# Optimization experiments

Measured on AMD Instinct MI355X. Metric: run time of the kernel, lower is better.

The kernel has to match this reference:

```python
import jax, jax.numpy as jnp
import numpy as np

NUM_HEADS = 16
D_MODEL = 1024
TEMPERATURE = D_MODEL ** 0.5  # note: module uses d_model**0.5, not head_dim**0.5


def setup_inputs() -> dict:
    key = jax.random.key(0)
    ks = jax.random.split(key, 8)
    B, T, D = 2, 2048, D_MODEL
    q = jax.random.normal(ks[0], (B, T, D), dtype=jnp.float32)
    k = jax.random.normal(ks[1], (B, T, D), dtype=jnp.float32)
    v = jax.random.normal(ks[2], (B, T, D), dtype=jnp.float32)
    # causal mask (tril) as suggested by the module docstring
    mask = jnp.tril(jnp.ones((T, T), dtype=bool))
    s = 1.0 / np.sqrt(D)
    Wq = jax.random.normal(ks[3], (D, D), dtype=jnp.float32) * s
    Wk = jax.random.normal(ks[4], (D, D), dtype=jnp.float32) * s
    Wv = jax.random.normal(ks[5], (D, D), dtype=jnp.float32) * s
    Wc = jax.random.normal(ks[6], (D, D), dtype=jnp.float32) * s
    return {"q": q, "k": k, "v": v, "Wq": Wq, "Wk": Wk, "Wv": Wv, "Wc": Wc, "mask": mask}


def reference(q, k, v, Wq, Wk, Wv, Wc, mask):
    B, T, D = q.shape
    H = NUM_HEADS
    hd = D // H
    # torch Linear (no bias): y = x @ W.T ; then split heads -> [B,H,T,hd]
    def proj(x, W):
        return (x @ W.T).reshape(B, T, H, hd).transpose(0, 2, 1, 3)
    qh, kh, vh = proj(q, Wq), proj(k, Wk), proj(v, Wv)
    # scores [B,H,T,T]
    scores = jnp.einsum("bhqd,bhkd->bhqk", qh / TEMPERATURE, kh)
    scores = jnp.where(mask, scores, -jnp.inf)
    attention = jax.nn.softmax(scores, axis=-1)  # dropout = identity (eval)
    out = jnp.einsum("bhqk,bhkd->bhqd", attention, vh)
    out = out.transpose(0, 2, 1, 3).reshape(B, T, D)
    out = out @ Wc.T  # combine projection; dropout = identity (eval)
    return (out, attention)
```

## Files before the change

kernel.cpp:

```cpp
#include <hip/hip_runtime.h>
#include <stdint.h>

typedef unsigned short u16;
typedef __bf16 bf16x8 __attribute__((ext_vector_type(8)));
typedef float f32x4 __attribute__((ext_vector_type(4)));

#define MFMA16(a, b, c) __builtin_amdgcn_mfma_f32_16x16x32_bf16((a), (b), (c), 0, 0, 0)

__device__ __forceinline__ u16 f2bf(float f) {
  union { __bf16 h; u16 u; } v;
  v.h = (__bf16)f;
  return v.u;
}

__device__ __forceinline__ float expf_c(float x) {
  return __expf(fmaxf(x, -80.0f));
}

__device__ __forceinline__ void gl_lds16(const u16* g, u16* l) {
  __builtin_amdgcn_global_load_lds(
      (const __attribute__((address_space(1))) unsigned int*)g,
      (__attribute__((address_space(3))) unsigned int*)l, 16, 0, 0);
}

struct Cvt6Args {
  const float* s0; const float* s1; const float* s2;
  const float* s3; const float* s4; const float* s5;
  u16* d0; u16* d1; u16* d2; u16* d3; u16* d4; u16* d5;
};

__global__ __launch_bounds__(256) void cvt6(Cvt6Args a) {
  const int z = blockIdx.y;
  const float* s; u16* d; int n8;
  if (z == 0)      { s = a.s0; d = a.d0; n8 = (4 * 1024 * 1024) / 8; }
  else if (z == 1) { s = a.s1; d = a.d1; n8 = (4 * 1024 * 1024) / 8; }
  else if (z == 2) { s = a.s2; d = a.d2; n8 = (4 * 1024 * 1024) / 8; }
  else if (z == 3) { s = a.s3; d = a.d3; n8 = (1024 * 1024) / 8; }
  else if (z == 4) { s = a.s4; d = a.d4; n8 = (1024 * 1024) / 8; }
  else             { s = a.s5; d = a.d5; n8 = (1024 * 1024) / 8; }
  const int i = blockIdx.x * 256 + threadIdx.x;
  if (i >= n8) return;
  float4 f0 = ((const float4*)s)[2 * i];
  float4 f1 = ((const float4*)s)[2 * i + 1];
  ushort4 h0, h1;
  h0.x = f2bf(f0.x); h0.y = f2bf(f0.y); h0.z = f2bf(f0.z); h0.w = f2bf(f0.w);
  h1.x = f2bf(f1.x); h1.y = f2bf(f1.y); h1.z = f2bf(f1.z); h1.w = f2bf(f1.w);
  ((ushort4*)d)[2 * i] = h0;
  ((ushort4*)d)[2 * i + 1] = h1;
}

__global__ __launch_bounds__(256) void cvt_one(const float* __restrict__ s,
                                               u16* __restrict__ d) {
  const int i = blockIdx.x * 256 + threadIdx.x;
  if (i >= (1024 * 1024) / 8) return;
  float4 f0 = ((const float4*)s)[2 * i];
  float4 f1 = ((const float4*)s)[2 * i + 1];
  ushort4 h0, h1;
  h0.x = f2bf(f0.x); h0.y = f2bf(f0.y); h0.z = f2bf(f0.z); h0.w = f2bf(f0.w);
  h1.x = f2bf(f1.x); h1.y = f2bf(f1.y); h1.z = f2bf(f1.z); h1.w = f2bf(f1.w);
  ((ushort4*)d)[2 * i] = h0;
  ((ushort4*)d)[2 * i + 1] = h1;
}

template <int BM>
__device__ __forceinline__ void gemm_core(const u16* __restrict__ X,
                                          const u16* __restrict__ W,
                                          void* __restrict__ Yv, float scale,
                                          int omode) {
  constexpr int NF = (BM == 128) ? 4 : 2;
  constexpr int ASEG = BM / 8;
  constexpr int CNT = (ASEG + 16) / 4;
  __shared__ __align__(16) u16 lA[BM * 64];
  __shared__ __align__(16) u16 lB[128 * 64];
  const int tid = threadIdx.x;
  const int lane = tid & 63, w = tid >> 6;
  const int l15 = lane & 15, quad = lane >> 4;
  const int wm = (BM == 128) ? (w >> 1) * 64 : 0;
  const int wn = (BM == 128) ? (w & 1) * 64 : w * 32;
  const int n0 = blockIdx.x * 128, m0 = blockIdx.y * BM;

  f32x4 acc[4][NF];
#pragma unroll
  for (int m = 0; m < 4; ++m)
#pragma unroll
    for (int n = 0; n < NF; ++n) acc[m][n] = (f32x4){0.f, 0.f, 0.f, 0.f};

  const int row8 = lane >> 3;
  const int slot = lane & 7;
  const int scol = ((slot ^ row8) << 3);

  for (int kk = 0; kk < 1024; kk += 64) {
    __syncthreads();
#pragma unroll
    for (int ps = 0; ps < CNT; ++ps) {
      const int s = w * CNT + ps;
      if (s < ASEG) {
        const int row = s * 8 + row8;
        gl_lds16(&X[(size_t)(m0 + row) * 1024 + kk + scol], &lA[s * 512]);
      } else {
        const int s2 = s - ASEG;
        const int row = s2 * 8 + row8;
        gl_lds16(&W[(size_t)(n0 + row) * 1024 + kk + scol], &lB[s2 * 512]);
      }
    }
    __syncthreads();
    bf16x8 af[2][4], bfr[2][NF];
#pragma unroll
    for (int h = 0; h < 2; ++h) {
#pragma unroll
      for (int m = 0; m < 4; ++m) {
        const int rA = wm + m * 16 + l15;
        af[h][m] = *(const bf16x8*)&lA[rA * 64 + (((quad + 4 * h) ^ (rA & 7)) << 3)];
      }
#pragma unroll
      for (int n = 0; n < NF; ++n) {
        const int rB = wn + n * 16 + l15;
        bfr[h][n] = *(const bf16x8*)&lB[rB * 64 + (((quad + 4 * h) ^ (rB & 7)) << 3)];
      }
    }
#pragma unroll
    for (int h = 0; h < 2; ++h)
#pragma unroll
      for (int m = 0; m < 4; ++m)
#pragma unroll
        for (int n = 0; n < NF; ++n)
          acc[m][n] = MFMA16(af[h][m], bfr[h][n], acc[m][n]);
  }

  if (omode == 0) {
    u16* Y = (u16*)Yv;
#pragma unroll
    for (int m = 0; m < 4; ++m) {
      int grow0 = m0 + wm + m * 16 + quad * 4;
#pragma unroll
      for (int n = 0; n < NF; ++n) {
        int gcol = n0 + wn + n * 16 + l15;
#pragma unroll
        for (int r = 0; r < 4; ++r)
          Y[(size_t)(grow0 + r) * 1024 + gcol] = f2bf(acc[m][n][r] * scale);
      }
    }
  } else if (omode == 1) {
    u16* Y = (u16*)Yv;
#pragma unroll
    for (int m = 0; m < 4; ++m) {
      int grow0 = m0 + wm + m * 16 + quad * 4;
      int bb = grow0 >> 11, t = grow0 & 2047;
#pragma unroll
      for (int n = 0; n < NF; ++n) {
        int gcol = n0 + wn + n * 16 + l15;
        int hh = gcol >> 6, e = gcol & 63;
        ushort4 pk;
        pk.x = f2bf(acc[m][n][0]);
        pk.y = f2bf(acc[m][n][1]);
        pk.z = f2bf(acc[m][n][2]);
        pk.w = f2bf(acc[m][n][3]);
        *(ushort4*)&Y[((size_t)((bb * 16 + hh) * 64 + e)) * 2048 + t] = pk;
      }
    }
  } else {
    float* Y = (float*)Yv;
#pragma unroll
    for (int m = 0; m < 4; ++m) {
      int grow0 = m0 + wm + m * 16 + quad * 4;
#pragma unroll
      for (int n = 0; n < NF; ++n) {
        int gcol = n0 + wn + n * 16 + l15;
#pragma unroll
        for (int r = 0; r < 4; ++r)
          Y[(size_t)(grow0 + r) * 1024 + gcol] = acc[m][n][r] * scale;
      }
    }
  }
}

struct QKVArgs {
  const u16* X0; const u16* X1; const u16* X2;
  const u16* W0; const u16* W1; const u16* W2;
  void* Y0; void* Y1; void* Y2;
  float s0, s1, s2;
};

__global__ __launch_bounds__(256, 2) void proj_qkv(QKVArgs a) {
  const u16* X; const u16* W; void* Y; float sc; int om;
  if (blockIdx.z == 0)      { X = a.X0; W = a.W0; Y = a.Y0; sc = a.s0; om = 0; }
  else if (blockIdx.z == 1) { X = a.X1; W = a.W1; Y = a.Y1; sc = a.s1; om = 0; }
  else                      { X = a.X2; W = a.W2; Y = a.Y2; sc = a.s2; om = 1; }
  gemm_core<64>(X, W, Y, sc, om);
}

__global__ __launch_bounds__(256, 2) void proj_out(const u16* __restrict__ Xv,
                                                   const u16* __restrict__ W,
                                                   void* __restrict__ Yv) {
  gemm_core<64>(Xv, W, Yv, 1.0f, 2);
}

__global__ __launch_bounds__(256, 4) void attn_kernel(const u16* __restrict__ Qb,
                                                      const u16* __restrict__ Kb,
                                                      const u16* __restrict__ Vt,
                                                      float* __restrict__ attnF,
                                                      u16* __restrict__ Ob) {
  __shared__ __align__(16) u16 lK[64 * 72];
  __shared__ __align__(16) u16 lV[64 * 72];
  __shared__ __align__(16) u16 lP[4][16 * 72];

  const int bid = blockIdx.x;
  const int qt = bid >> 5;
  const int bh = bid & 31;
  const int b = bh >> 4, h = bh & 15;
  const int q0 = qt * 64;
  const int tid = threadIdx.x;
  const int w = tid >> 6, lane = tid & 63;
  const int l15 = lane & 15, quad = lane >> 4;
  const f32x4 ZERO4 = {0.f, 0.f, 0.f, 0.f};

  {
    const int kz0 = q0 + 64;
    if (kz0 < 2048) {
      for (int r = w; r < 64; r += 4) {
        size_t base = ((size_t)bh * 2048 + q0 + r) * 2048;
        uint4 z = {0, 0, 0, 0};
        for (int c = kz0 + lane * 4; c < 2048; c += 256)
          *(uint4*)&attnF[base + c] = z;
      }
    }
  }

  const int qrow = q0 + w * 16 + l15;
  const size_t qrowbase = (size_t)(b * 2048 + qrow) * 1024 + h * 64;
  const bf16x8 aq0 = *(const bf16x8*)&Qb[qrowbase + quad * 8];
  const bf16x8 aq1 = *(const bf16x8*)&Qb[qrowbase + 32 + quad * 8];

  const int kq = quad * 4;
  const int srow = tid >> 3, sseg = (tid & 7) * 8;

  float lacc = 0.f;
  for (int c = 0; c <= qt; ++c) {
    const int k0 = c * 64;
    __syncthreads();
#pragma unroll
    for (int p = 0; p < 2; ++p) {
      int rr = p * 32 + srow;
      *(uint4*)&lK[rr * 72 + sseg] =
          *(const uint4*)&Kb[(size_t)(b * 2048 + k0 + rr) * 1024 + h * 64 + sseg];
    }
    __syncthreads();
#pragma unroll
    for (int n = 0; n < 4; ++n) {
      bf16x8 bk0 = *(const bf16x8*)&lK[(n * 16 + l15) * 72 + quad * 8];
      bf16x8 bk1 = *(const bf16x8*)&lK[(n * 16 + l15) * 72 + 32 + quad * 8];
      f32x4 s = MFMA16(bk0, aq0, ZERO4);
      s = MFMA16(bk1, aq1, s);
      const int keyb = k0 + n * 16 + kq;
      if (c == qt) {
#pragma unroll
        for (int i = 0; i < 4; ++i)
          lacc += (keyb + i > qrow) ? 0.f : expf_c(s[i]);
      } else {
#pragma unroll
        for (int i = 0; i < 4; ++i) lacc += expf_c(s[i]);
      }
    }
  }
  lacc += __shfl_xor(lacc, 16);
  lacc += __shfl_xor(lacc, 32);
  const float invl = 1.0f / fmaxf(lacc, 1e-30f);

  f32x4 o[4];
#pragma unroll
  for (int n = 0; n < 4; ++n) o[n] = ZERO4;
  const size_t arow = ((size_t)bh * 2048 + qrow) * 2048;
  u16* lPw = lP[w];

  for (int c = 0; c <= qt; ++c) {
    const int k0 = c * 64;
    __syncthreads();
#pragma unroll
    for (int p = 0; p < 2; ++p) {
      int rr = p * 32 + srow;
      *(uint4*)&lK[rr * 72 + sseg] =
          *(const uint4*)&Kb[(size_t)(b * 2048 + k0 + rr) * 1024 + h * 64 + sseg];
      *(uint4*)&lV[rr * 72 + sseg] =
          *(const uint4*)&Vt[((size_t)bh * 64 + rr) * 2048 + k0 + sseg];
    }
    __syncthreads();
    const bool diag = (c == qt);
#pragma unroll
    for (int n = 0; n < 4; ++n) {
      bf16x8 bk0 = *(const bf16x8*)&lK[(n * 16 + l15) * 72 + quad * 8];
      bf16x8 bk1 = *(const bf16x8*)&lK[(n * 16 + l15) * 72 + 32 + quad * 8];
      f32x4 s = MFMA16(bk0, aq0, ZERO4);
      s = MFMA16(bk1, aq1, s);
      const int keyb = k0 + n * 16 + kq;
#pragma unroll
      for (int i = 0; i < 4; ++i) {
        float pv = expf_c(s[i]) * invl;
        if (diag && keyb + i > qrow) pv = 0.f;
        s[i] = pv;
      }
      *(f32x4*)&attnF[arow + keyb] = s;
      ushort4 pk;
      pk.x = f2bf(s[0]); pk.y = f2bf(s[1]); pk.z = f2bf(s[2]); pk.w = f2bf(s[3]);
      *(ushort4*)&lPw[l15 * 72 + n * 16 + kq] = pk;
    }
#pragma unroll
    for (int kkk = 0; kkk < 2; ++kkk) {
      bf16x8 ap = *(const bf16x8*)&lPw[l15 * 72 + kkk * 32 + quad * 8];
#pragma unroll
      for (int n = 0; n < 4; ++n) {
        bf16x8 bv = *(const bf16x8*)&lV[(n * 16 + l15) * 72 + kkk * 32 + quad * 8];
        o[n] = MFMA16(ap, bv, o[n]);
      }
    }
  }

#pragma unroll
  for (int n = 0; n < 4; ++n)
#pragma unroll
    for (int i = 0; i < 4; ++i) {
      float ov = o[n][i];
      if (!(ov == ov)) ov = 0.f;
      lPw[(quad * 4 + i) * 72 + n * 16 + l15] = f2bf(ov);
    }
  {
    int prow = lane >> 3, pseg = (lane & 7) * 8;
#pragma unroll
    for (int p2 = 0; p2 < 2; ++p2) {
      int rr = p2 * 8 + prow;
      *(uint4*)&Ob[(size_t)(b * 2048 + q0 + w * 16 + rr) * 1024 + h * 64 + pseg] =
          *(const uint4*)&lPw[rr * 72 + pseg];
    }
  }
}

extern "C" void kernel_launch(void* const* d_in, const int* in_sizes, int n_in,
                              void* d_out, int out_size, void* d_ws, size_t ws_size,
                              hipStream_t stream) {
  const float* q  = (const float*)d_in[0];
  const float* k  = (const float*)d_in[1];
  const float* v  = (const float*)d_in[2];
  const float* Wq = (const float*)d_in[3];
  const float* Wk = (const float*)d_in[4];
  const float* Wv = (const float*)d_in[5];
  const float* Wc = (const float*)d_in[6];

  float* outF  = (float*)d_out;
  float* attnF = outF + (size_t)4096 * 1024;

  const size_t BUF  = (size_t)4096 * 1024;
  const size_t WBUF = (size_t)1024 * 1024;
  u16* ws = (u16*)d_ws;
  const bool big_ws = ws_size >= 4 * BUF * sizeof(u16);

  u16 *Qb, *Kb, *Vt, *Ob;
  if (big_ws) {
    Qb = ws; Kb = ws + BUF; Vt = ws + 2 * BUF; Ob = ws + 3 * BUF;
  } else {
    Qb = (u16*)outF; Ob = (u16*)outF + BUF; Kb = ws; Vt = ws + BUF;
  }

  u16* qbf  = (u16*)attnF;
  u16* kbf  = qbf  + BUF;
  u16* vbf  = kbf  + BUF;
  u16* wqbf = vbf  + BUF;
  u16* wkbf = wqbf + WBUF;
  u16* wvbf = wkbf + WBUF;
  u16* wcbf = Vt;

  dim3 blk(256, 1, 1);

  Cvt6Args ca;
  ca.s0 = q;    ca.s1 = k;    ca.s2 = v;
  ca.s3 = Wq;   ca.s4 = Wk;   ca.s5 = Wv;
  ca.d0 = qbf;  ca.d1 = kbf;  ca.d2 = vbf;
  ca.d3 = wqbf; ca.d4 = wkbf; ca.d5 = wvbf;
  cvt6<<<dim3(2048, 6), blk, 0, stream>>>(ca);

  QKVArgs a;
  a.X0 = qbf;  a.X1 = kbf;  a.X2 = vbf;
  a.W0 = wqbf; a.W1 = wkbf; a.W2 = wvbf;
  a.Y0 = Qb; a.Y1 = Kb; a.Y2 = Vt;
  a.s0 = 0.03125f;
  a.s1 = 1.0f; a.s2 = 1.0f;
  proj_qkv<<<dim3(8, 64, 3), blk, 0, stream>>>(a);
  attn_kernel<<<dim3(1024), blk, 0, stream>>>(Qb, Kb, Vt, attnF, Ob);

  cvt_one<<<dim3(512), blk, 0, stream>>>(Wc, wcbf);

  const u16* gemm_src = Ob;
  if (!big_ws) {
    (void)hipMemcpyAsync(ws, Ob, BUF * sizeof(u16), hipMemcpyDeviceToDevice, stream);
    gemm_src = ws;
  }
  proj_out<<<dim3(8, 64), blk, 0, stream>>>(gemm_src, wcbf, outF);
}
```

Measured before the change: 738.1 us.

## Double-buffer K/V tiles in attention with register prefetch

The attention kernel's K and V LDS tiles become double buffers. The next tile's global loads are issued into registers before computing on the current tile, then written into the other buffer, so each iteration needs one barrier instead of two. This is meant to hide global load latency behind MFMA and exp work. LDS use doubles, extra registers hold the prefetched data, and launch bounds drop from 4 to 3 blocks per CU, which may lower occupancy.

```diff
diff --git a/kernel.cpp b/kernel.cpp
--- a/kernel.cpp
+++ b/kernel.cpp
@@ -195,13 +195,13 @@
   gemm_core<64>(Xv, W, Yv, 1.0f, 2);
 }
 
-__global__ __launch_bounds__(256, 4) void attn_kernel(const u16* __restrict__ Qb,
+__global__ __launch_bounds__(256, 3) void attn_kernel(const u16* __restrict__ Qb,
                                                       const u16* __restrict__ Kb,
                                                       const u16* __restrict__ Vt,
                                                       float* __restrict__ attnF,
                                                       u16* __restrict__ Ob) {
-  __shared__ __align__(16) u16 lK[64 * 72];
-  __shared__ __align__(16) u16 lV[64 * 72];
+  __shared__ __align__(16) u16 lK[2][64 * 72];
+  __shared__ __align__(16) u16 lV[2][64 * 72];
   __shared__ __align__(16) u16 lP[4][16 * 72];
 
   const int bid = blockIdx.x;
@@ -233,22 +233,29 @@
 
   const int kq = quad * 4;
   const int srow = tid >> 3, sseg = (tid & 7) * 8;
+  const size_t kbase = (size_t)b * 2048 * 1024 + h * 64 + sseg;
+  const size_t vbase = (size_t)bh * 64 * 2048 + sseg;
 
   float lacc = 0.f;
+  {
+    uint4 a0 = *(const uint4*)&Kb[kbase + (size_t)srow * 1024];
+    uint4 a1 = *(const uint4*)&Kb[kbase + (size_t)(32 + srow) * 1024];
+    *(uint4*)&lK[0][srow * 72 + sseg] = a0;
+    *(uint4*)&lK[0][(32 + srow) * 72 + sseg] = a1;
+  }
+  __syncthreads();
   for (int c = 0; c <= qt; ++c) {
-    const int k0 = c * 64;
-    __syncthreads();
-#pragma unroll
-    for (int p = 0; p < 2; ++p) {
-      int rr = p * 32 + srow;
-      *(uint4*)&lK[rr * 72 + sseg] =
-          *(const uint4*)&Kb[(size_t)(b * 2048 + k0 + rr) * 1024 + h * 64 + sseg];
-    }
-    __syncthreads();
+    const int k0 = c * 64, cur = c & 1;
+    const bool pf = (c < qt);
+    uint4 p0, p1;
+    if (pf) {
+      p0 = *(const uint4*)&Kb[kbase + (size_t)(k0 + 64 + srow) * 1024];
+      p1 = *(const uint4*)&Kb[kbase + (size_t)(k0 + 96 + srow) * 1024];
+    }
 #pragma unroll
     for (int n = 0; n < 4; ++n) {
-      bf16x8 bk0 = *(const bf16x8*)&lK[(n * 16 + l15) * 72 + quad * 8];
-      bf16x8 bk1 = *(const bf16x8*)&lK[(n * 16 + l15) * 72 + 32 + quad * 8];
+      bf16x8 bk0 = *(const bf16x8*)&lK[cur][(n * 16 + l15) * 72 + quad * 8];
+      bf16x8 bk1 = *(const bf16x8*)&lK[cur][(n * 16 + l15) * 72 + 32 + quad * 8];
       f32x4 s = MFMA16(bk0, aq0, ZERO4);
       s = MFMA16(bk1, aq1, s);
       const int keyb = k0 + n * 16 + kq;
@@ -261,6 +268,11 @@
         for (int i = 0; i < 4; ++i) lacc += expf_c(s[i]);
       }
     }
+    if (pf) {
+      *(uint4*)&lK[cur ^ 1][srow * 72 + sseg] = p0;
+      *(uint4*)&lK[cur ^ 1][(32 + srow) * 72 + sseg] = p1;
+    }
+    __syncthreads();
   }
   lacc += __shfl_xor(lacc, 16);
   lacc += __shfl_xor(lacc, 32);
@@ -272,23 +284,32 @@
   const size_t arow = ((size_t)bh * 2048 + qrow) * 2048;
   u16* lPw = lP[w];
 
+  {
+    uint4 a0 = *(const uint4*)&Kb[kbase + (size_t)srow * 1024];
+    uint4 a1 = *(const uint4*)&Kb[kbase + (size_t)(32 + srow) * 1024];
+    uint4 b0 = *(const uint4*)&Vt[vbase + (size_t)srow * 2048];
+    uint4 b1 = *(const uint4*)&Vt[vbase + (size_t)(32 + srow) * 2048];
+    *(uint4*)&lK[0][srow * 72 + sseg] = a0;
+    *(uint4*)&lK[0][(32 + srow) * 72 + sseg] = a1;
+    *(uint4*)&lV[0][srow * 72 + sseg] = b0;
+    *(uint4*)&lV[0][(32 + srow) * 72 + sseg] = b1;
+  }
+  __syncthreads();
   for (int c = 0; c <= qt; ++c) {
-    const int k0 = c * 64;
-    __syncthreads();
-#pragma unroll
-    for (int p = 0; p < 2; ++p) {
-      int rr = p * 32 + srow;
-      *(uint4*)&lK[rr * 72 + sseg] =
-          *(const uint4*)&Kb[(size_t)(b * 2048 + k0 + rr) * 1024 + h * 64 + sseg];
-      *(uint4*)&lV[rr * 72 + sseg] =
-          *(const uint4*)&Vt[((size_t)bh * 64 + rr) * 2048 + k0 + sseg];
-    }
-    __syncthreads();
+    const int k0 = c * 64, cur = c & 1;
+    const bool pf = (c < qt);
+    uint4 p0, p1, v0, v1;
+    if (pf) {
+      p0 = *(const uint4*)&Kb[kbase + (size_t)(k0 + 64 + srow) * 1024];
+      p1 = *(const uint4*)&Kb[kbase + (size_t)(k0 + 96 + srow) * 1024];
+      v0 = *(const uint4*)&Vt[vbase + (size_t)srow * 2048 + k0 + 64];
+      v1 = *(const uint4*)&Vt[vbase + (size_t)(32 + srow) * 2048 + k0 + 64];
+    }
     const bool diag = (c == qt);
 #pragma unroll
     for (int n = 0; n < 4; ++n) {
-      bf16x8 bk0 = *(const bf16x8*)&lK[(n * 16 + l15) * 72 + quad * 8];
-      bf16x8 bk1 = *(const bf16x8*)&lK[(n * 16 + l15) * 72 + 32 + quad * 8];
+      bf16x8 bk0 = *(const bf16x8*)&lK[cur][(n * 16 + l15) * 72 + quad * 8];
+      bf16x8 bk1 = *(const bf16x8*)&lK[cur][(n * 16 + l15) * 72 + 32 + quad * 8];
       f32x4 s = MFMA16(bk0, aq0, ZERO4);
       s = MFMA16(bk1, aq1, s);
       const int keyb = k0 + n * 16 + kq;
@@ -308,10 +329,17 @@
       bf16x8 ap = *(const bf16x8*)&lPw[l15 * 72 + kkk * 32 + quad * 8];
 #pragma unroll
       for (int n = 0; n < 4; ++n) {
-        bf16x8 bv = *(const bf16x8*)&lV[(n * 16 + l15) * 72 + kkk * 32 + quad * 8];
+        bf16x8 bv = *(const bf16x8*)&lV[cur][(n * 16 + l15) * 72 + kkk * 32 + quad * 8];
         o[n] = MFMA16(ap, bv, o[n]);
       }
     }
+    if (pf) {
+      *(uint4*)&lK[cur ^ 1][srow * 72 + sseg] = p0;
+      *(uint4*)&lK[cur ^ 1][(32 + srow) * 72 + sseg] = p1;
+      *(uint4*)&lV[cur ^ 1][srow * 72 + sseg] = v0;
+      *(uint4*)&lV[cur ^ 1][(32 + srow) * 72 + sseg] = v1;
+    }
+    __syncthreads();
   }
 
 #pragma unroll
```

Result: no change. 727.8 us (-1.4%).
